# Optimization experiments

Measured on AMD Instinct MI355X. Metric: run time of the kernel, lower is better.

## Reference

```python
import jax, jax.numpy as jnp
import numpy as np

N_NODES = 50000


def gcn_conv(x, edge_index, W, b, n):
    # x: [N, F_in]; edge_index: [2, E] (src, dst)
    h = x @ W  # [N, F_out]
    loops = jnp.arange(n, dtype=edge_index.dtype)
    src = jnp.concatenate([edge_index[0], loops])
    dst = jnp.concatenate([edge_index[1], loops])
    # symmetric normalization: deg^{-1/2}[src] * deg^{-1/2}[dst]
    deg = jax.ops.segment_sum(jnp.ones_like(src, dtype=h.dtype), dst, num_segments=n)
    dinv = jnp.where(deg > 0, jax.lax.rsqrt(deg), 0.0)
    norm = dinv[src] * dinv[dst]  # [E+N]
    msg = h[src] * norm[:, None]  # gather + scale
    out = jax.ops.segment_sum(msg, dst, num_segments=n)  # scatter-add
    return out + b


def setup_inputs() -> dict:
    key = jax.random.key(0)
    k1, k2, k3, k4 = jax.random.split(key, 4)
    x = jax.random.normal(k1, (N_NODES, 1433), dtype=jnp.float32)
    edge_index = jax.random.randint(k2, (2, 1600000), 0, N_NODES, dtype=jnp.int64)
    W1 = jax.random.normal(k3, (1433, 16), dtype=jnp.float32) * 0.05
    b1 = jnp.zeros((16,), dtype=jnp.float32)
    W2 = jax.random.normal(k4, (16, 7), dtype=jnp.float32) * 0.2
    b2 = jnp.zeros((7,), dtype=jnp.float32)
    return {"x": x, "edge_index": edge_index, "W1": W1, "b1": b1, "W2": W2, "b2": b2}


def reference(x, edge_index, W1, b1, W2, b2):
    n = x.shape[0]
    h = gcn_conv(x, edge_index, W1, b1, n)
    h = jax.nn.relu(h)
    # dropout is identity in eval mode
    h = gcn_conv(h, edge_index, W2, b2, n)
    return jax.nn.log_softmax(h, axis=1)
```

## Files before the change

kernel.cpp:

```cpp
#include <hip/hip_runtime.h>
#include <math.h>

#define F_IN 1433
#define F1 16
#define F2 7
#define SCAN_CHUNK 2048
#define NREP 8
#define NSEG1 4
#define KSEG1 360

__global__ void k_init_cnt(int* __restrict__ cnt_r, int n) {
    int i = blockIdx.x * 256 + threadIdx.x;
    if (i < n) cnt_r[i] = 0;
}

__global__ void k_count(const int* __restrict__ edges, int* __restrict__ cnt_r,
                        int E, int N) {
    int e = blockIdx.x * 256 + threadIdx.x;
    if (e < E) atomicAdd(&cnt_r[(blockIdx.x & (NREP - 1)) * N + edges[E + e]], 1);
}

__global__ void k_scan1(const int* __restrict__ cnt_r, int* __restrict__ rs,
                        int* __restrict__ bsum, int N) {
    __shared__ int sh[256];
    int tid = threadIdx.x;
    int base = blockIdx.x * SCAN_CHUNK + tid * 8;
    int v[8];
    int s = 0;
#pragma unroll
    for (int u = 0; u < 8; ++u) {
        int idx = base + u;
        int t = 0;
        if (idx < N) {
#pragma unroll
            for (int r = 0; r < NREP; ++r) t += cnt_r[r * N + idx];
        }
        v[u] = t;
        s += t;
    }
    sh[tid] = s;
    __syncthreads();
    for (int off = 1; off < 256; off <<= 1) {
        int y = 0;
        if (tid >= off) y = sh[tid - off];
        __syncthreads();
        sh[tid] += y;
        __syncthreads();
    }
    int run = sh[tid] - s;
#pragma unroll
    for (int u = 0; u < 8; ++u) {
        int idx = base + u;
        if (idx < N) rs[idx] = run;
        run += v[u];
    }
    if (tid == 255) bsum[blockIdx.x] = sh[255];
}

__global__ void k_scan2(const int* __restrict__ bsum, int* __restrict__ boff, int NB) {
    if (blockIdx.x == 0 && threadIdx.x == 0) {
        int r = 0;
        for (int b = 0; b < NB; ++b) { int t = bsum[b]; boff[b] = r; r += t; }
    }
}

__global__ void k_scan3(int* __restrict__ rs, int* __restrict__ cursor_r,
                        const int* __restrict__ cnt_r, int* __restrict__ cnt,
                        float* __restrict__ dinv, const int* __restrict__ boff, int N) {
    int i = blockIdx.x * 256 + threadIdx.x;
    if (i < N) {
        int run = rs[i] + boff[i / SCAN_CHUNK];
        rs[i] = run;
        int total = 0;
#pragma unroll
        for (int r = 0; r < NREP; ++r) {
            cursor_r[r * N + i] = run;
            int c = cnt_r[r * N + i];
            run += c;
            total += c;
        }
        cnt[i] = total;
        dinv[i] = rsqrtf((float)total + 1.0f);
    }
}

__global__ void k_fill(const int* __restrict__ edges, int* __restrict__ cursor_r,
                       int* __restrict__ col, int E, int N) {
    int e = blockIdx.x * 256 + threadIdx.x;
    if (e < E) {
        int d = edges[E + e];
        int s = edges[e];
        int pos = atomicAdd(&cursor_r[(blockIdx.x & (NREP - 1)) * N + d], 1);
        col[pos] = s;
    }
}

__device__ __forceinline__ void fma16(float acc[16], float xm,
                                      const float* __restrict__ wr) {
    const float4* w4 = (const float4*)wr;
    float4 w0 = w4[0], w1 = w4[1], w2 = w4[2], w3 = w4[3];
    acc[0]  = fmaf(xm, w0.x, acc[0]);  acc[1]  = fmaf(xm, w0.y, acc[1]);
    acc[2]  = fmaf(xm, w0.z, acc[2]);  acc[3]  = fmaf(xm, w0.w, acc[3]);
    acc[4]  = fmaf(xm, w1.x, acc[4]);  acc[5]  = fmaf(xm, w1.y, acc[5]);
    acc[6]  = fmaf(xm, w1.z, acc[6]);  acc[7]  = fmaf(xm, w1.w, acc[7]);
    acc[8]  = fmaf(xm, w2.x, acc[8]);  acc[9]  = fmaf(xm, w2.y, acc[9]);
    acc[10] = fmaf(xm, w2.z, acc[10]); acc[11] = fmaf(xm, w2.w, acc[11]);
    acc[12] = fmaf(xm, w3.x, acc[12]); acc[13] = fmaf(xm, w3.y, acc[13]);
    acc[14] = fmaf(xm, w3.z, acc[14]); acc[15] = fmaf(xm, w3.w, acc[15]);
}

__device__ __forceinline__ void fma_grp32(float acc[16], const float4 cur[8],
                                          const float* __restrict__ W, int kbase) {
#pragma unroll
    for (int i = 0; i < 8; ++i) {
        const float* wr = W + (kbase + i * 4) * 16;
        fma16(acc, cur[i].x, wr);
        fma16(acc, cur[i].y, wr + 16);
        fma16(acc, cur[i].z, wr + 32);
        fma16(acc, cur[i].w, wr + 48);
    }
}

__global__ __launch_bounds__(64) void k_gemv1(const float* __restrict__ x,
                                              const float* __restrict__ W,
                                              float* __restrict__ gpart, int N) {
    const int g   = blockIdx.x;
    const int seg = blockIdx.y;
    const int par = g & 3;
    const int l   = threadIdx.x;
    int row = (g >> 2) * 256 + par + 4 * l;
    const bool ok = row < N;
    if (!ok) row = ((N - 1 - par) & ~3) + par;

    const int k0 = seg * KSEG1;
    const int k1 = min(k0 + KSEG1, F_IN);
    const int sh = (4 - ((par + k0) & 3)) & 3;
    const float* xr = x + (long)row * F_IN;

    float acc[16];
#pragma unroll
    for (int j = 0; j < 16; ++j) acc[j] = 0.f;

    for (int m = 0; m < sh; ++m) {
        float xv = xr[k0 + m];
        fma16(acc, xv, W + (k0 + m) * 16);
    }

    const int kb   = k0 + sh;
    const int kcnt = k1 - kb;
    const int ng   = kcnt >> 5;
    const float4* xp = (const float4*)(xr + kb);

    if (ng > 0) {
        float4 cur[8];
#pragma unroll
        for (int i = 0; i < 8; ++i) cur[i] = xp[i];
        for (int c = 0; c < ng - 1; ++c) {
            float4 nxt[8];
            const float4* q = xp + (c + 1) * 8;
#pragma unroll
            for (int i = 0; i < 8; ++i) nxt[i] = q[i];
            fma_grp32(acc, cur, W, kb + c * 32);
#pragma unroll
            for (int i = 0; i < 8; ++i) cur[i] = nxt[i];
        }
        fma_grp32(acc, cur, W, kb + (ng - 1) * 32);
    }

    const int k4b = kb + (ng << 5);
    const int n4  = (k1 - k4b) >> 2;
    for (int c = 0; c < n4; ++c) {
        const int k = k4b + (c << 2);
        const float4 xv = *(const float4*)(xr + k);
        const float* wr = W + k * 16;
        fma16(acc, xv.x, wr);
        fma16(acc, xv.y, wr + 16);
        fma16(acc, xv.z, wr + 32);
        fma16(acc, xv.w, wr + 48);
    }

    for (int k = k4b + (n4 << 2); k < k1; ++k) {
        float xv = xr[k];
        fma16(acc, xv, W + k * 16);
    }

    if (ok) {
        float4* o = (float4*)(gpart + ((long)seg * N + row) * 16);
        o[0] = make_float4(acc[0],  acc[1],  acc[2],  acc[3]);
        o[1] = make_float4(acc[4],  acc[5],  acc[6],  acc[7]);
        o[2] = make_float4(acc[8],  acc[9],  acc[10], acc[11]);
        o[3] = make_float4(acc[12], acc[13], acc[14], acc[15]);
    }
}

__global__ __launch_bounds__(256) void k_greduce(const float* __restrict__ gpart,
                                                 const float* __restrict__ dinv,
                                                 float* __restrict__ g, int N, int nseg) {
    int i4 = blockIdx.x * 256 + threadIdx.x;
    if (i4 >= N * 4) return;
    const float4* gp = (const float4*)gpart;
    float4 s = gp[i4];
    for (int p = 1; p < nseg; ++p) {
        float4 t = gp[(long)p * N * 4 + i4];
        s.x += t.x; s.y += t.y; s.z += t.z; s.w += t.w;
    }
    float d = dinv[i4 >> 2];
    s.x *= d; s.y *= d; s.z *= d; s.w *= d;
    ((float4*)g)[i4] = s;
}

__global__ __launch_bounds__(256) void k_gather1(const int* __restrict__ col,
                                                 const int* __restrict__ rs,
                                                 const int* __restrict__ cnt,
                                                 const float* __restrict__ g,
                                                 const float* __restrict__ dinv,
                                                 const float* __restrict__ b1,
                                                 float* __restrict__ x1, int N) {
    int node = blockIdx.x * 4 + (threadIdx.x >> 6);
    if (node >= N) return;
    int lane = threadIdx.x & 63;
    int q = lane >> 4;
    int j = lane & 15;
    int start = rs[node];
    int c = cnt[node];
    float acc = 0.f;
    int p = q;
    if (p < c) {
        int s = col[start + p];
        for (;;) {
            int pn = p + 4;
            bool more = pn < c;
            int sn = 0;
            if (more) sn = col[start + pn];
            acc += g[(long)s * F1 + j];
            if (!more) break;
            s = sn; p = pn;
        }
    }
    acc += __shfl_down(acc, 32, 64);
    acc += __shfl_down(acc, 16, 64);
    if (lane < 16) {
        float v = dinv[node] * (acc + g[(long)node * F1 + j]) + b1[j];
        x1[(long)node * F1 + j] = fmaxf(v, 0.f);
    }
}

__global__ __launch_bounds__(256) void k_gemm2(const float* __restrict__ x1,
                                               const float* __restrict__ W2,
                                               const float* __restrict__ dinv,
                                               float* __restrict__ g2, int N) {
    int i = blockIdx.x * 256 + threadIdx.x;
    if (i >= N) return;
    const float4* xr = (const float4*)(x1 + (long)i * F1);
    float4 a0 = xr[0], a1 = xr[1], a2 = xr[2], a3 = xr[3];
    float xv[F1] = {a0.x, a0.y, a0.z, a0.w, a1.x, a1.y, a1.z, a1.w,
                    a2.x, a2.y, a2.z, a2.w, a3.x, a3.y, a3.z, a3.w};
    float acc[F2];
#pragma unroll
    for (int j = 0; j < F2; ++j) acc[j] = 0.f;
#pragma unroll
    for (int k = 0; k < F1; ++k) {
#pragma unroll
        for (int j = 0; j < F2; ++j) acc[j] = fmaf(xv[k], W2[k * F2 + j], acc[j]);
    }
    float d = dinv[i];
    float4* out = (float4*)(g2 + (long)i * 8);
    out[0] = make_float4(d * acc[0], d * acc[1], d * acc[2], d * acc[3]);
    out[1] = make_float4(d * acc[4], d * acc[5], d * acc[6], 0.f);
}

__global__ __launch_bounds__(256) void k_gather2(const int* __restrict__ col,
                                                 const int* __restrict__ rs,
                                                 const int* __restrict__ cnt,
                                                 const float* __restrict__ g2,
                                                 const float* __restrict__ dinv,
                                                 const float* __restrict__ b2,
                                                 float* __restrict__ out, int N) {
    int node = blockIdx.x * 4 + (threadIdx.x >> 6);
    if (node >= N) return;
    int lane = threadIdx.x & 63;
    int q = lane >> 3;
    int j = lane & 7;
    int start = rs[node];
    int c = cnt[node];
    float acc = 0.f;
    int p = q;
    if (p < c) {
        int s = col[start + p];
        for (;;) {
            int pn = p + 8;
            bool more = pn < c;
            int sn = 0;
            if (more) sn = col[start + pn];
            acc += g2[(long)s * 8 + j];
            if (!more) break;
            s = sn; p = pn;
        }
    }
    acc += __shfl_down(acc, 32, 64);
    acc += __shfl_down(acc, 16, 64);
    acc += __shfl_down(acc, 8, 64);
    if (lane < 8) {
        float vv = -INFINITY;
        if (j < F2)
            vv = dinv[node] * (acc + g2[(long)node * 8 + j]) + b2[j];
        float m = vv;
        m = fmaxf(m, __shfl_xor(m, 1, 64));
        m = fmaxf(m, __shfl_xor(m, 2, 64));
        m = fmaxf(m, __shfl_xor(m, 4, 64));
        float e = (j < F2) ? expf(vv - m) : 0.f;
        e += __shfl_xor(e, 1, 64);
        e += __shfl_xor(e, 2, 64);
        e += __shfl_xor(e, 4, 64);
        if (j < F2)
            out[(long)node * F2 + j] = vv - m - logf(e);
    }
}

extern "C" void kernel_launch(void* const* d_in, const int* in_sizes, int n_in,
                              void* d_out, int out_size, void* d_ws, size_t ws_size,
                              hipStream_t stream) {
    const float* x     = (const float*)d_in[0];
    const int*   edges = (const int*)d_in[1];
    const float* W1    = (const float*)d_in[2];
    const float* b1    = (const float*)d_in[3];
    const float* W2    = (const float*)d_in[4];
    const float* b2    = (const float*)d_in[5];
    float* outp = (float*)d_out;

    int N = in_sizes[0] / F_IN;
    int E = in_sizes[1] / 2;
    int NB = (N + SCAN_CHUNK - 1) / SCAN_CHUNK;

    char* ws = (char*)d_ws;
    size_t o = 0;
    auto alloc = [&](size_t bytes) { size_t r = o; o += (bytes + 255) & ~(size_t)255; return r; };
    int*   cnt_r    = (int*)  (ws + alloc((size_t)NREP * N * 4));
    int*   cursor_r = (int*)  (ws + alloc((size_t)NREP * N * 4));
    int*   cnt      = (int*)  (ws + alloc((size_t)N * 4));
    int*   rs       = (int*)  (ws + alloc((size_t)N * 4));
    float* dinv     = (float*)(ws + alloc((size_t)N * 4));
    int*   bsum     = (int*)  (ws + alloc((size_t)NB * 4));
    int*   boff     = (int*)  (ws + alloc((size_t)NB * 4));
    int*   col      = (int*)  (ws + alloc((size_t)E * 4));
    float* g        = (float*)(ws + alloc((size_t)N * F1 * 4));
    float* x1       = (float*)(ws + alloc((size_t)N * F1 * 4));
    float* g2       = (float*)(ws + alloc((size_t)N * 8 * 4));
    float* gpart    = (float*)(ws + alloc((size_t)NSEG1 * N * F1 * 4));
    (void)n_in; (void)out_size; (void)ws_size;

    int gN256 = (N + 255) / 256;
    int gE256 = (E + 255) / 256;

    k_init_cnt<<<(NREP * N + 255) / 256, 256, 0, stream>>>(cnt_r, NREP * N);
    k_count<<<gE256, 256, 0, stream>>>(edges, cnt_r, E, N);
    k_scan1<<<NB, 256, 0, stream>>>(cnt_r, rs, bsum, N);
    k_scan2<<<1, 64, 0, stream>>>(bsum, boff, NB);
    k_scan3<<<gN256, 256, 0, stream>>>(rs, cursor_r, cnt_r, cnt, dinv, boff, N);
    k_fill<<<gE256, 256, 0, stream>>>(edges, cursor_r, col, E, N);

    int NG = (N + 255) / 256;
    dim3 g1(NG * 4, NSEG1);
    k_gemv1<<<g1, 64, 0, stream>>>(x, W1, gpart, N);
    k_greduce<<<(N * 4 + 255) / 256, 256, 0, stream>>>(gpart, dinv, g, N, NSEG1);
    k_gather1<<<(N + 3) / 4, 256, 0, stream>>>(col, rs, cnt, g, dinv, b1, x1, N);
    k_gemm2<<<gN256, 256, 0, stream>>>(x1, W2, dinv, g2, N);
    k_gather2<<<(N + 3) / 4, 256, 0, stream>>>(col, rs, cnt, g2, dinv, b2, outp, N);
}
```

Baseline: 676.6 us.

## Restructure first-layer GEMV to K-split lanes with register-resident weights and shuffle reduction

The first-layer x@W1 kernel now assigns each lane a strided slice of the K dimension and keeps its 6x16 slice of W1 in registers, instead of giving each lane a full row. Each wave then processes 64 rows two at a time, so x reads are coalesced across lanes, and the 16 partial outputs are reduced with a butterfly of cross-lane shuffles. Loads for upcoming row pairs are software-pipelined three deep. The aim is to replace strided per-row x reads with coalesced ones and drop repeated W1 loads. The cost is a large register footprint and many shuffles per row pair, and the K segment length changes to 384.

```diff
diff --git a/kernel.cpp b/kernel.cpp
--- a/kernel.cpp
+++ b/kernel.cpp
@@ -7,7 +7,7 @@
 #define SCAN_CHUNK 2048
 #define NREP 8
 #define NSEG1 4
-#define KSEG1 360
+#define KSEG1 384
 
 __global__ void k_init_cnt(int* __restrict__ cnt_r, int n) {
     int i = blockIdx.x * 256 + threadIdx.x;
@@ -95,102 +95,105 @@
     }
 }
 
-__device__ __forceinline__ void fma16(float acc[16], float xm,
-                                      const float* __restrict__ wr) {
-    const float4* w4 = (const float4*)wr;
-    float4 w0 = w4[0], w1 = w4[1], w2 = w4[2], w3 = w4[3];
-    acc[0]  = fmaf(xm, w0.x, acc[0]);  acc[1]  = fmaf(xm, w0.y, acc[1]);
-    acc[2]  = fmaf(xm, w0.z, acc[2]);  acc[3]  = fmaf(xm, w0.w, acc[3]);
-    acc[4]  = fmaf(xm, w1.x, acc[4]);  acc[5]  = fmaf(xm, w1.y, acc[5]);
-    acc[6]  = fmaf(xm, w1.z, acc[6]);  acc[7]  = fmaf(xm, w1.w, acc[7]);
-    acc[8]  = fmaf(xm, w2.x, acc[8]);  acc[9]  = fmaf(xm, w2.y, acc[9]);
-    acc[10] = fmaf(xm, w2.z, acc[10]); acc[11] = fmaf(xm, w2.w, acc[11]);
-    acc[12] = fmaf(xm, w3.x, acc[12]); acc[13] = fmaf(xm, w3.y, acc[13]);
-    acc[14] = fmaf(xm, w3.z, acc[14]); acc[15] = fmaf(xm, w3.w, acc[15]);
-}
-
-__device__ __forceinline__ void fma_grp32(float acc[16], const float4 cur[8],
-                                          const float* __restrict__ W, int kbase) {
-#pragma unroll
-    for (int i = 0; i < 8; ++i) {
-        const float* wr = W + (kbase + i * 4) * 16;
-        fma16(acc, cur[i].x, wr);
-        fma16(acc, cur[i].y, wr + 16);
-        fma16(acc, cur[i].z, wr + 32);
-        fma16(acc, cur[i].w, wr + 48);
+template <int S>
+__device__ __forceinline__ void bstep(float b[32], int sub) {
+#pragma unroll
+    for (int m = 0; m < S; ++m) {
+        bool up = (sub & S) != 0;
+        float keep = up ? b[m + S] : b[m];
+        float send = up ? b[m] : b[m + S];
+        b[m] = keep + __shfl_xor(send, S, 64);
+    }
+}
+
+__device__ __forceinline__ void load_pair(const float* __restrict__ x, int row0,
+                                          int kl, int N, float xc0[6], float xc1[6]) {
+    const float* p0 = x + (long)row0 * F_IN + kl;
+#pragma unroll
+    for (int t = 0; t < 6; ++t) {
+        int k = kl + 64 * t;
+        bool kk = k < F_IN;
+        xc0[t] = (kk && row0 < N)     ? p0[64 * t]        : 0.f;
+        xc1[t] = (kk && row0 + 1 < N) ? p0[F_IN + 64 * t] : 0.f;
+    }
+}
+
+__device__ __forceinline__ void comp_pair(const float wreg[6][16],
+                                          const float xc0[6], const float xc1[6],
+                                          int row0, int sub, int lane,
+                                          long segbase, int N,
+                                          float* __restrict__ gpart) {
+    float b[32];
+#pragma unroll
+    for (int j = 0; j < 16; ++j) {
+        b[j]      = xc0[0] * wreg[0][j];
+        b[16 + j] = xc1[0] * wreg[0][j];
+    }
+#pragma unroll
+    for (int t = 1; t < 6; ++t) {
+#pragma unroll
+        for (int j = 0; j < 16; ++j) {
+            b[j]      = fmaf(xc0[t], wreg[t][j], b[j]);
+            b[16 + j] = fmaf(xc1[t], wreg[t][j], b[16 + j]);
+        }
+    }
+#pragma unroll
+    for (int m = 0; m < 32; ++m) b[m] += __shfl_xor(b[m], 32, 64);
+    bstep<16>(b, sub);
+    bstep<8>(b, sub);
+    bstep<4>(b, sub);
+    bstep<2>(b, sub);
+    bstep<1>(b, sub);
+    if (lane < 32) {
+        int row = row0 + (sub >> 4);
+        if (row < N) gpart[segbase + (long)row * 16 + (sub & 15)] = b[0];
     }
 }
 
 __global__ __launch_bounds__(64) void k_gemv1(const float* __restrict__ x,
                                               const float* __restrict__ W,
                                               float* __restrict__ gpart, int N) {
-    const int g   = blockIdx.x;
-    const int seg = blockIdx.y;
-    const int par = g & 3;
-    const int l   = threadIdx.x;
-    int row = (g >> 2) * 256 + par + 4 * l;
-    const bool ok = row < N;
-    if (!ok) row = ((N - 1 - par) & ~3) + par;
-
-    const int k0 = seg * KSEG1;
-    const int k1 = min(k0 + KSEG1, F_IN);
-    const int sh = (4 - ((par + k0) & 3)) & 3;
-    const float* xr = x + (long)row * F_IN;
-
-    float acc[16];
-#pragma unroll
-    for (int j = 0; j < 16; ++j) acc[j] = 0.f;
-
-    for (int m = 0; m < sh; ++m) {
-        float xv = xr[k0 + m];
-        fma16(acc, xv, W + (k0 + m) * 16);
-    }
-
-    const int kb   = k0 + sh;
-    const int kcnt = k1 - kb;
-    const int ng   = kcnt >> 5;
-    const float4* xp = (const float4*)(xr + kb);
-
-    if (ng > 0) {
-        float4 cur[8];
-#pragma unroll
-        for (int i = 0; i < 8; ++i) cur[i] = xp[i];
-        for (int c = 0; c < ng - 1; ++c) {
-            float4 nxt[8];
-            const float4* q = xp + (c + 1) * 8;
-#pragma unroll
-            for (int i = 0; i < 8; ++i) nxt[i] = q[i];
-            fma_grp32(acc, cur, W, kb + c * 32);
-#pragma unroll
-            for (int i = 0; i < 8; ++i) cur[i] = nxt[i];
-        }
-        fma_grp32(acc, cur, W, kb + (ng - 1) * 32);
-    }
-
-    const int k4b = kb + (ng << 5);
-    const int n4  = (k1 - k4b) >> 2;
-    for (int c = 0; c < n4; ++c) {
-        const int k = k4b + (c << 2);
-        const float4 xv = *(const float4*)(xr + k);
-        const float* wr = W + k * 16;
-        fma16(acc, xv.x, wr);
-        fma16(acc, xv.y, wr + 16);
-        fma16(acc, xv.z, wr + 32);
-        fma16(acc, xv.w, wr + 48);
-    }
-
-    for (int k = k4b + (n4 << 2); k < k1; ++k) {
-        float xv = xr[k];
-        fma16(acc, xv, W + k * 16);
-    }
-
-    if (ok) {
-        float4* o = (float4*)(gpart + ((long)seg * N + row) * 16);
-        o[0] = make_float4(acc[0],  acc[1],  acc[2],  acc[3]);
-        o[1] = make_float4(acc[4],  acc[5],  acc[6],  acc[7]);
-        o[2] = make_float4(acc[8],  acc[9],  acc[10], acc[11]);
-        o[3] = make_float4(acc[12], acc[13], acc[14], acc[15]);
-    }
+    const int lane = threadIdx.x;
+    const int seg  = blockIdx.y;
+    const int k0   = seg * KSEG1;
+    const int r0   = blockIdx.x * 64;
+    const int kl   = k0 + lane;
+    const int sub  = lane & 31;
+    const long segbase = (long)seg * N * 16;
+
+    float wreg[6][16];
+#pragma unroll
+    for (int t = 0; t < 6; ++t) {
+        int k = kl + 64 * t;
+        if (k < F_IN) {
+            const float4* wr = (const float4*)(W + (long)k * 16);
+            float4 a = wr[0], b4 = wr[1], c = wr[2], d = wr[3];
+            wreg[t][0]  = a.x;  wreg[t][1]  = a.y;  wreg[t][2]  = a.z;  wreg[t][3]  = a.w;
+            wreg[t][4]  = b4.x; wreg[t][5]  = b4.y; wreg[t][6]  = b4.z; wreg[t][7]  = b4.w;
+            wreg[t][8]  = c.x;  wreg[t][9]  = c.y;  wreg[t][10] = c.z;  wreg[t][11] = c.w;
+            wreg[t][12] = d.x;  wreg[t][13] = d.y;  wreg[t][14] = d.z;  wreg[t][15] = d.w;
+        } else {
+#pragma unroll
+            for (int j = 0; j < 16; ++j) wreg[t][j] = 0.f;
+        }
+    }
+
+    float A0[6], A1[6], B0[6], B1[6], C0[6], C1[6];
+    load_pair(x, r0 + 0, kl, N, A0, A1);
+    load_pair(x, r0 + 2, kl, N, B0, B1);
+    load_pair(x, r0 + 4, kl, N, C0, C1);
+
+#pragma unroll 1
+    for (int p = 0; p < 30; p += 3) {
+        comp_pair(wreg, A0, A1, r0 + 2 * p, sub, lane, segbase, N, gpart);
+        if (p + 3 < 32) load_pair(x, r0 + 2 * (p + 3), kl, N, A0, A1);
+        comp_pair(wreg, B0, B1, r0 + 2 * (p + 1), sub, lane, segbase, N, gpart);
+        if (p + 4 < 32) load_pair(x, r0 + 2 * (p + 4), kl, N, B0, B1);
+        comp_pair(wreg, C0, C1, r0 + 2 * (p + 2), sub, lane, segbase, N, gpart);
+        if (p + 5 < 32) load_pair(x, r0 + 2 * (p + 5), kl, N, C0, C1);
+    }
+    comp_pair(wreg, A0, A1, r0 + 60, sub, lane, segbase, N, gpart);
+    comp_pair(wreg, B0, B1, r0 + 62, sub, lane, segbase, N, gpart);
 }
 
 __global__ __launch_bounds__(256) void k_greduce(const float* __restrict__ gpart,
@@ -359,8 +362,8 @@
     k_scan3<<<gN256, 256, 0, stream>>>(rs, cursor_r, cnt_r, cnt, dinv, boff, N);
     k_fill<<<gE256, 256, 0, stream>>>(edges, cursor_r, col, E, N);
 
-    int NG = (N + 255) / 256;
-    dim3 g1(NG * 4, NSEG1);
+    int RB = (N + 63) / 64;
+    dim3 g1(RB, NSEG1);
     k_gemv1<<<g1, 64, 0, stream>>>(x, W1, gpart, N);
     k_greduce<<<(N * 4 + 255) / 256, 256, 0, stream>>>(gpart, dinv, g, N, NSEG1);
     k_gather1<<<(N + 3) / 4, 256, 0, stream>>>(col, rs, cnt, g, dinv, b1, x1, N);
```

New measurement: 699.0 us. 1.03x slower.
